# Kernel tuning notes

Hardware: AMD Instinct MI355X
Metric: run time of the kernel (lower is better)

The kernel has to match this reference:

```python
import jax, jax.numpy as jnp
import numpy as np

B, S, E, H, D = 384, 128, 512, 4, 128  # batch, seq(block), embed, heads, head_dim


def setup_inputs() -> dict:
    key = jax.random.key(0)
    ks = jax.random.split(key, 6)
    scale = 1.0 / np.sqrt(E)  # lecun_normal-ish fan-in scaling
    return {
        "x": jax.random.normal(ks[0], (B, S, E), dtype=jnp.float32),
        "Wq": jax.random.normal(ks[1], (E, E), dtype=jnp.float32) * scale,
        "bq": jnp.zeros((E,), dtype=jnp.float32),
        "Wk": jax.random.normal(ks[2], (E, E), dtype=jnp.float32) * scale,
        "bk": jnp.zeros((E,), dtype=jnp.float32),
        "Wv": jax.random.normal(ks[3], (E, E), dtype=jnp.float32) * scale,
        "bv": jnp.zeros((E,), dtype=jnp.float32),
        "Wo": jax.random.normal(ks[4], (E, E), dtype=jnp.float32) * scale,
        "bo": jnp.zeros((E,), dtype=jnp.float32),
    }


def reference(x, Wq, bq, Wk, bk, Wv, bv, Wo, bo):
    # Projections, then split heads: [B,S,E] -> [B,S,H,D]
    q = (x @ Wq + bq).reshape(B, S, H, D)
    k = (x @ Wk + bk).reshape(B, S, H, D)
    v = (x @ Wv + bv).reshape(B, S, H, D)
    # NOTE: original applies no 1/sqrt(D) scaling and no mask.
    scores = jnp.einsum("BSHD,BTHD->BHST", q, k)  # [B,H,S,T]
    weights = jax.nn.softmax(scores, axis=-1)
    out = jnp.einsum("BHST,BTHD->BSHD", weights, v).reshape(B, S, E)
    return out @ Wo + bo
```

## Files before the change

kernel.cpp:

```cpp
#include <hip/hip_runtime.h>
#include <hip/hip_bf16.h>
#include <cstdint>


#define EMB 512

typedef __attribute__((ext_vector_type(4))) float    f32x4;
typedef __attribute__((ext_vector_type(8))) _Float16 f16x8;

#define MFMA16(a, b, c) __builtin_amdgcn_mfma_f32_16x16x32_f16((a), (b), (c), 0, 0, 0)

__device__ __forceinline__ int swz128(int row, int col) {
    return row * 128 + (col ^ (((row >> 2) & 3) << 4));
}
__device__ __forceinline__ int swz64(int row, int col) {
    return row * 64 + (col ^ (((row >> 2) & 3) << 4));
}

__device__ __forceinline__ void gld_lds16(const _Float16* g, _Float16* l) {
    __builtin_amdgcn_global_load_lds(
        (const __attribute__((address_space(1))) void*)g,
        (__attribute__((address_space(3))) void*)l, 16, 0, 0);
}

__device__ __forceinline__ void stage64(_Float16* lds, const _Float16* gbase,
                                        int grow0, int k0, int wave, int lane) {
#pragma unroll
    for (int i = 0; i < 4; ++i) {
        int idx = wave * 256 + i * 64 + lane;
        int n   = idx >> 3;
        int kb  = (idx & 7) ^ (((n >> 2) & 3) << 1);
        gld_lds16(gbase + (grow0 + n) * EMB + k0 + kb * 8,
                  lds + wave * 2048 + i * 512);
    }
}

__device__ __forceinline__ void proj_gemm(f32x4 acc[2][8],
        const _Float16* __restrict__ abase, int arow0,
        const _Float16* __restrict__ sbase, int srow0,
        _Float16* stageL, int wave, int lane) {
    const int l15 = lane & 15, quad = lane >> 4;
    for (int k0 = 0; k0 < EMB; k0 += 64) {
        stage64(stageL, sbase, srow0, k0, wave, lane);
        __syncthreads();
#pragma unroll
        for (int ktl = 0; ktl < 2; ++ktl) {
            int kk = k0 + ktl * 32 + quad * 8;
            f16x8 a0 = *(const f16x8*)(abase + (arow0 + l15) * EMB + kk);
            f16x8 a1 = *(const f16x8*)(abase + (arow0 + 16 + l15) * EMB + kk);
#pragma unroll
            for (int nt = 0; nt < 8; ++nt) {
                int n = nt * 16 + l15;
                int c = (ktl * 32 + quad * 8) ^ (((n >> 2) & 3) << 4);
                f16x8 bb = *(const f16x8*)(stageL + n * 64 + c);
                acc[0][nt] = MFMA16(a0, bb, acc[0][nt]);
                acc[1][nt] = MFMA16(a1, bb, acc[1][nt]);
            }
        }
        __syncthreads();
    }
}

#define ZACC(A)                                   \
    _Pragma("unroll") for (int _i = 0; _i < 2; ++_i) \
    _Pragma("unroll") for (int _j = 0; _j < 8; ++_j) \
        A[_i][_j] = (f32x4){0.f, 0.f, 0.f, 0.f};

__global__ void k_cvt_x(const float* __restrict__ x, _Float16* __restrict__ xh) {
    long i = ((long)blockIdx.x * 256 + threadIdx.x) * 8;
    f32x4 a = *(const f32x4*)(x + i);
    f32x4 b = *(const f32x4*)(x + i + 4);
    f16x8 o;
    o[0] = (_Float16)a[0]; o[1] = (_Float16)a[1];
    o[2] = (_Float16)a[2]; o[3] = (_Float16)a[3];
    o[4] = (_Float16)b[0]; o[5] = (_Float16)b[1];
    o[6] = (_Float16)b[2]; o[7] = (_Float16)b[3];
    *(f16x8*)(xh + i) = o;
}

__global__ void k_transpose_w(const float* __restrict__ W, _Float16* __restrict__ Wt) {
    __shared__ float t[32][33];
    int tid = threadIdx.x;
    int tx = tid & 31, ty = tid >> 5;
    int k0 = blockIdx.x * 32, n0 = blockIdx.y * 32;
#pragma unroll
    for (int i = 0; i < 4; ++i)
        t[ty + i * 8][tx] = W[(k0 + ty + i * 8) * EMB + n0 + tx];
    __syncthreads();
#pragma unroll
    for (int i = 0; i < 4; ++i)
        Wt[(n0 + ty + i * 8) * EMB + k0 + tx] = (_Float16)t[tx][ty + i * 8];
}

__global__ __launch_bounds__(256, 2)
void k_attn(const _Float16* __restrict__ xh,
            const _Float16* __restrict__ Wqt, const _Float16* __restrict__ Wkt,
            const _Float16* __restrict__ Wvt,
            const float* __restrict__ bq, const float* __restrict__ bk,
            const float* __restrict__ bv,
            _Float16* __restrict__ attn) {
    __shared__ _Float16 RA[128 * 128];
    __shared__ _Float16 RB[128 * 128];
    const int tid = threadIdx.x, wave = tid >> 6, lane = tid & 63;
    const int l15 = lane & 15, quad = lane >> 4;
    const int b = blockIdx.x >> 2, h = blockIdx.x & 3;
    const int sRow0 = b * 128, wRow0 = h * 128;
    f32x4 acc[2][8];

    ZACC(acc);
    proj_gemm(acc, xh, sRow0 + wave * 32, Wqt, wRow0, RB, wave, lane);
#pragma unroll
    for (int mt = 0; mt < 2; ++mt)
#pragma unroll
        for (int nt = 0; nt < 8; ++nt) {
            int col = nt * 16 + l15;
            float bias = bq[wRow0 + col];
#pragma unroll
            for (int r = 0; r < 4; ++r) {
                int row = wave * 32 + mt * 16 + quad * 4 + r;
                RA[swz128(row, col)] = (_Float16)(acc[mt][nt][r] + bias);
            }
        }

    ZACC(acc);
    proj_gemm(acc, xh, sRow0 + wave * 32, Wkt, wRow0, RB, wave, lane);
#pragma unroll
    for (int mt = 0; mt < 2; ++mt)
#pragma unroll
        for (int nt = 0; nt < 8; ++nt) {
            int col = nt * 16 + l15;
            float bias = bk[wRow0 + col];
#pragma unroll
            for (int r = 0; r < 4; ++r) {
                int row = wave * 32 + mt * 16 + quad * 4 + r;
                RB[swz128(row, col)] = (_Float16)(acc[mt][nt][r] + bias);
            }
        }
    __syncthreads();

    ZACC(acc);
#pragma unroll
    for (int kt = 0; kt < 4; ++kt) {
        int ca = kt * 32 + quad * 8;
        int rq = wave * 32 + l15;
        f16x8 q0 = *(const f16x8*)&RA[swz128(rq, ca)];
        f16x8 q1 = *(const f16x8*)&RA[swz128(rq + 16, ca)];
#pragma unroll
        for (int nt = 0; nt < 8; ++nt) {
            f16x8 kf = *(const f16x8*)&RB[swz128(nt * 16 + l15, ca)];
            acc[0][nt] = MFMA16(q0, kf, acc[0][nt]);
            acc[1][nt] = MFMA16(q1, kf, acc[1][nt]);
        }
    }
#pragma unroll
    for (int mt = 0; mt < 2; ++mt)
#pragma unroll
        for (int r = 0; r < 4; ++r) {
            float mx = acc[mt][0][r];
#pragma unroll
            for (int nt = 1; nt < 8; ++nt) mx = fmaxf(mx, acc[mt][nt][r]);
            mx = fmaxf(mx, __shfl_xor(mx, 1));
            mx = fmaxf(mx, __shfl_xor(mx, 2));
            mx = fmaxf(mx, __shfl_xor(mx, 4));
            mx = fmaxf(mx, __shfl_xor(mx, 8));
            float sm = 0.f;
#pragma unroll
            for (int nt = 0; nt < 8; ++nt) {
                float e = __expf(acc[mt][nt][r] - mx);
                acc[mt][nt][r] = e;
                sm += e;
            }
            sm += __shfl_xor(sm, 1);
            sm += __shfl_xor(sm, 2);
            sm += __shfl_xor(sm, 4);
            sm += __shfl_xor(sm, 8);
            float inv = 1.0f / sm;
#pragma unroll
            for (int nt = 0; nt < 8; ++nt) acc[mt][nt][r] *= inv;
        }
    __syncthreads();

#pragma unroll
    for (int mt = 0; mt < 2; ++mt)
#pragma unroll
        for (int nt = 0; nt < 8; ++nt) {
            int col = nt * 16 + l15;
#pragma unroll
            for (int r = 0; r < 4; ++r) {
                int row = wave * 32 + mt * 16 + quad * 4 + r;
                RA[swz128(row, col)] = (_Float16)acc[mt][nt][r];
            }
        }

    ZACC(acc);
    proj_gemm(acc, Wvt, wRow0 + wave * 32, xh, sRow0, RB, wave, lane);
#pragma unroll
    for (int mt = 0; mt < 2; ++mt)
#pragma unroll
        for (int r = 0; r < 4; ++r) {
            int row = wave * 32 + mt * 16 + quad * 4 + r;
            float bias = bv[wRow0 + row];
#pragma unroll
            for (int nt = 0; nt < 8; ++nt) {
                int col = nt * 16 + l15;
                RB[swz128(row, col)] = (_Float16)(acc[mt][nt][r] + bias);
            }
        }
    __syncthreads();

    ZACC(acc);
#pragma unroll
    for (int kt = 0; kt < 4; ++kt) {
        int ca = kt * 32 + quad * 8;
        int rp = wave * 32 + l15;
        f16x8 p0 = *(const f16x8*)&RA[swz128(rp, ca)];
        f16x8 p1 = *(const f16x8*)&RA[swz128(rp + 16, ca)];
#pragma unroll
        for (int nt = 0; nt < 8; ++nt) {
            f16x8 vf = *(const f16x8*)&RB[swz128(nt * 16 + l15, ca)];
            acc[0][nt] = MFMA16(p0, vf, acc[0][nt]);
            acc[1][nt] = MFMA16(p1, vf, acc[1][nt]);
        }
    }
    __syncthreads();

#pragma unroll
    for (int mt = 0; mt < 2; ++mt)
#pragma unroll
        for (int nt = 0; nt < 8; ++nt) {
            int col = nt * 16 + l15;
#pragma unroll
            for (int r = 0; r < 4; ++r) {
                int row = wave * 32 + mt * 16 + quad * 4 + r;
                RA[swz128(row, col)] = (_Float16)acc[mt][nt][r];
            }
        }
    __syncthreads();
#pragma unroll
    for (int i = 0; i < 8; ++i) {
        int idx = i * 256 + tid;
        int row = idx >> 4, col = (idx & 15) * 8;
        f16x8 v = *(const f16x8*)&RA[row * 128 + (col ^ (((row >> 2) & 3) << 4))];
        *(f16x8*)(attn + (long)(sRow0 + row) * EMB + wRow0 + col) = v;
    }
}

__global__ __launch_bounds__(256, 3)
void k_out(const _Float16* __restrict__ attn, const _Float16* __restrict__ Wot,
           const float* __restrict__ bo, float* __restrict__ out) {
    __shared__ _Float16 SA[128 * 64];
    __shared__ _Float16 SB[128 * 64];
    const int tid = threadIdx.x, wave = tid >> 6, lane = tid & 63;
    const int l15 = lane & 15, quad = lane >> 4;
    const int m0 = (blockIdx.x >> 2) * 128, n0 = (blockIdx.x & 3) * 128;
    f32x4 acc[2][8];
    ZACC(acc);
    for (int k0 = 0; k0 < EMB; k0 += 64) {
        stage64(SA, attn, m0, k0, wave, lane);
        stage64(SB, Wot, n0, k0, wave, lane);
        __syncthreads();
#pragma unroll
        for (int ktl = 0; ktl < 2; ++ktl) {
            int ra = wave * 32 + l15;
            int cb = ktl * 32 + quad * 8;
            f16x8 a0 = *(const f16x8*)&SA[swz64(ra, cb)];
            f16x8 a1 = *(const f16x8*)&SA[swz64(ra + 16, cb)];
#pragma unroll
            for (int nt = 0; nt < 8; ++nt) {
                f16x8 bb = *(const f16x8*)&SB[swz64(nt * 16 + l15, cb)];
                acc[0][nt] = MFMA16(a0, bb, acc[0][nt]);
                acc[1][nt] = MFMA16(a1, bb, acc[1][nt]);
            }
        }
        __syncthreads();
    }
#pragma unroll
    for (int nt = 0; nt < 8; ++nt) {
        int col = n0 + nt * 16 + l15;
        float bias = bo[col];
#pragma unroll
        for (int mt = 0; mt < 2; ++mt)
#pragma unroll
            for (int r = 0; r < 4; ++r) {
                int row = m0 + wave * 32 + mt * 16 + quad * 4 + r;
                out[(long)row * EMB + col] = acc[mt][nt][r] + bias;
            }
    }
}

extern "C" void kernel_launch(void* const* d_in, const int* in_sizes, int n_in,
                              void* d_out, int out_size, void* d_ws, size_t ws_size,
                              hipStream_t stream) {
    const float* x  = (const float*)d_in[0];
    const float* Wq = (const float*)d_in[1];
    const float* bq = (const float*)d_in[2];
    const float* Wk = (const float*)d_in[3];
    const float* bk = (const float*)d_in[4];
    const float* Wv = (const float*)d_in[5];
    const float* bv = (const float*)d_in[6];
    const float* Wo = (const float*)d_in[7];
    const float* bo = (const float*)d_in[8];
    float* out = (float*)d_out;

    _Float16* xh   = (_Float16*)d_ws;
    _Float16* Wqt  = (_Float16*)((char*)d_ws + 50331648);
    _Float16* Wkt  = Wqt + 262144;
    _Float16* Wvt  = Wkt + 262144;
    _Float16* Wot  = Wvt + 262144;
    _Float16* attn = Wot + 262144;

    k_cvt_x<<<12288, 256, 0, stream>>>(x, xh);
    dim3 tg(16, 16);
    k_transpose_w<<<tg, 256, 0, stream>>>(Wq, Wqt);
    k_transpose_w<<<tg, 256, 0, stream>>>(Wk, Wkt);
    k_transpose_w<<<tg, 256, 0, stream>>>(Wv, Wvt);
    k_transpose_w<<<tg, 256, 0, stream>>>(Wo, Wot);
    k_attn<<<1536, 256, 0, stream>>>(xh, Wqt, Wkt, Wvt, bq, bk, bv, attn);
    k_out<<<1536, 256, 0, stream>>>(attn, Wot, bo, out);
}
```

Baseline: 411.3 us.

## Split fused attention into a standalone QKV GEMM kernel and an attention-core kernel

Moves the Q/K/V projections out of the fused attention kernel into a separate GEMM kernel over a concatenated QKV weight. That kernel stages both operands in LDS and writes Q and K row-major and V transposed per head to global scratch. The attention core then only loads K and V^T tiles into LDS, reads Q from global, and does the softmax and PV. The old fused kernel read the A operand straight from global and ran serialized per-head projections. The split adds a round trip of Q/K/V through HBM (about 150MB) and an extra launch. It also raises k_out's occupancy hint to 4.

```diff
diff --git a/kernel.cpp b/kernel.cpp
--- a/kernel.cpp
+++ b/kernel.cpp
@@ -35,29 +35,16 @@
     }
 }
 
-__device__ __forceinline__ void proj_gemm(f32x4 acc[2][8],
-        const _Float16* __restrict__ abase, int arow0,
-        const _Float16* __restrict__ sbase, int srow0,
-        _Float16* stageL, int wave, int lane) {
-    const int l15 = lane & 15, quad = lane >> 4;
-    for (int k0 = 0; k0 < EMB; k0 += 64) {
-        stage64(stageL, sbase, srow0, k0, wave, lane);
-        __syncthreads();
-#pragma unroll
-        for (int ktl = 0; ktl < 2; ++ktl) {
-            int kk = k0 + ktl * 32 + quad * 8;
-            f16x8 a0 = *(const f16x8*)(abase + (arow0 + l15) * EMB + kk);
-            f16x8 a1 = *(const f16x8*)(abase + (arow0 + 16 + l15) * EMB + kk);
-#pragma unroll
-            for (int nt = 0; nt < 8; ++nt) {
-                int n = nt * 16 + l15;
-                int c = (ktl * 32 + quad * 8) ^ (((n >> 2) & 3) << 4);
-                f16x8 bb = *(const f16x8*)(stageL + n * 64 + c);
-                acc[0][nt] = MFMA16(a0, bb, acc[0][nt]);
-                acc[1][nt] = MFMA16(a1, bb, acc[1][nt]);
-            }
-        }
-        __syncthreads();
+__device__ __forceinline__ void stage128(_Float16* lds, const _Float16* gbase,
+                                         long grow0, int gstride, int gcol0,
+                                         int wave, int lane) {
+#pragma unroll
+    for (int i = 0; i < 8; ++i) {
+        int idx = wave * 512 + i * 64 + lane;
+        int n   = idx >> 4;
+        int kb  = (idx & 15) ^ (((n >> 2) & 3) << 1);
+        gld_lds16(gbase + (grow0 + n) * gstride + gcol0 + kb * 8,
+                  lds + wave * 4096 + i * 512);
     }
 }
 
@@ -92,62 +79,102 @@
         Wt[(n0 + ty + i * 8) * EMB + k0 + tx] = (_Float16)t[tx][ty + i * 8];
 }
 
+__global__ __launch_bounds__(256, 4)
+void k_qkv(const _Float16* __restrict__ xh, const _Float16* __restrict__ Wqkvt,
+           const float* __restrict__ bq, const float* __restrict__ bk,
+           const float* __restrict__ bv,
+           _Float16* __restrict__ qb, _Float16* __restrict__ kb,
+           _Float16* __restrict__ vtb) {
+    __shared__ _Float16 SA[128 * 64];
+    __shared__ _Float16 SB[128 * 64];
+    const int tid = threadIdx.x, wave = tid >> 6, lane = tid & 63;
+    const int l15 = lane & 15, quad = lane >> 4;
+    const int bi = blockIdx.x;
+    const int bb = bi / 12, j = bi - bb * 12;
+    const int m0 = bb * 128;
+    const bool vswap = (j >= 8);
+    const _Float16* As = vswap ? SB : SA;
+    const _Float16* Bs = vswap ? SA : SB;
+    f32x4 acc[2][8];
+    ZACC(acc);
+    for (int k0 = 0; k0 < EMB; k0 += 64) {
+        stage64(SA, xh, m0, k0, wave, lane);
+        stage64(SB, Wqkvt, j * 128, k0, wave, lane);
+        __syncthreads();
+#pragma unroll
+        for (int ktl = 0; ktl < 2; ++ktl) {
+            int cb = ktl * 32 + quad * 8;
+            f16x8 a0 = *(const f16x8*)&As[swz64(wave * 32 + l15, cb)];
+            f16x8 a1 = *(const f16x8*)&As[swz64(wave * 32 + 16 + l15, cb)];
+#pragma unroll
+            for (int nt = 0; nt < 8; ++nt) {
+                f16x8 bbf = *(const f16x8*)&Bs[swz64(nt * 16 + l15, cb)];
+                acc[0][nt] = MFMA16(a0, bbf, acc[0][nt]);
+                acc[1][nt] = MFMA16(a1, bbf, acc[1][nt]);
+            }
+        }
+        __syncthreads();
+    }
+    if (!vswap) {
+        const float* bias = (j < 4) ? bq : bk;
+        _Float16* dst = (j < 4) ? qb : kb;
+        const int nc0 = (j & 3) * 128;
+#pragma unroll
+        for (int nt = 0; nt < 8; ++nt) {
+            int col = nt * 16 + l15;
+            float bv_ = bias[nc0 + col];
+#pragma unroll
+            for (int mt = 0; mt < 2; ++mt)
+#pragma unroll
+                for (int r = 0; r < 4; ++r) {
+                    int row = wave * 32 + mt * 16 + quad * 4 + r;
+                    dst[(long)(m0 + row) * EMB + nc0 + col] =
+                        (_Float16)(acc[mt][nt][r] + bv_);
+                }
+        }
+    } else {
+        const int hv = j - 8;
+        _Float16* dst = vtb + (long)(bb * 4 + hv) * 128 * 128;
+#pragma unroll
+        for (int mt = 0; mt < 2; ++mt)
+#pragma unroll
+            for (int r = 0; r < 4; ++r) {
+                int d = wave * 32 + mt * 16 + quad * 4 + r;
+                float bvv = bv[hv * 128 + d];
+#pragma unroll
+                for (int nt = 0; nt < 8; ++nt) {
+                    int t = nt * 16 + l15;
+                    dst[d * 128 + t] = (_Float16)(acc[mt][nt][r] + bvv);
+                }
+            }
+    }
+}
+
 __global__ __launch_bounds__(256, 2)
-void k_attn(const _Float16* __restrict__ xh,
-            const _Float16* __restrict__ Wqt, const _Float16* __restrict__ Wkt,
-            const _Float16* __restrict__ Wvt,
-            const float* __restrict__ bq, const float* __restrict__ bk,
-            const float* __restrict__ bv,
-            _Float16* __restrict__ attn) {
-    __shared__ _Float16 RA[128 * 128];
-    __shared__ _Float16 RB[128 * 128];
+void k_core(const _Float16* __restrict__ qb, const _Float16* __restrict__ kb,
+            const _Float16* __restrict__ vtb, _Float16* __restrict__ attn) {
+    __shared__ _Float16 SK[128 * 128];
+    __shared__ _Float16 SV[128 * 128];
     const int tid = threadIdx.x, wave = tid >> 6, lane = tid & 63;
     const int l15 = lane & 15, quad = lane >> 4;
     const int b = blockIdx.x >> 2, h = blockIdx.x & 3;
     const int sRow0 = b * 128, wRow0 = h * 128;
     f32x4 acc[2][8];
 
-    ZACC(acc);
-    proj_gemm(acc, xh, sRow0 + wave * 32, Wqt, wRow0, RB, wave, lane);
-#pragma unroll
-    for (int mt = 0; mt < 2; ++mt)
-#pragma unroll
-        for (int nt = 0; nt < 8; ++nt) {
-            int col = nt * 16 + l15;
-            float bias = bq[wRow0 + col];
-#pragma unroll
-            for (int r = 0; r < 4; ++r) {
-                int row = wave * 32 + mt * 16 + quad * 4 + r;
-                RA[swz128(row, col)] = (_Float16)(acc[mt][nt][r] + bias);
-            }
-        }
-
-    ZACC(acc);
-    proj_gemm(acc, xh, sRow0 + wave * 32, Wkt, wRow0, RB, wave, lane);
-#pragma unroll
-    for (int mt = 0; mt < 2; ++mt)
-#pragma unroll
-        for (int nt = 0; nt < 8; ++nt) {
-            int col = nt * 16 + l15;
-            float bias = bk[wRow0 + col];
-#pragma unroll
-            for (int r = 0; r < 4; ++r) {
-                int row = wave * 32 + mt * 16 + quad * 4 + r;
-                RB[swz128(row, col)] = (_Float16)(acc[mt][nt][r] + bias);
-            }
-        }
+    stage128(SK, kb, sRow0, EMB, wRow0, wave, lane);
+    stage128(SV, vtb, (long)(b * 4 + h) * 128, 128, 0, wave, lane);
     __syncthreads();
 
     ZACC(acc);
 #pragma unroll
     for (int kt = 0; kt < 4; ++kt) {
         int ca = kt * 32 + quad * 8;
-        int rq = wave * 32 + l15;
-        f16x8 q0 = *(const f16x8*)&RA[swz128(rq, ca)];
-        f16x8 q1 = *(const f16x8*)&RA[swz128(rq + 16, ca)];
-#pragma unroll
-        for (int nt = 0; nt < 8; ++nt) {
-            f16x8 kf = *(const f16x8*)&RB[swz128(nt * 16 + l15, ca)];
+        const _Float16* qrow = qb + (long)(sRow0 + wave * 32 + l15) * EMB + wRow0 + ca;
+        f16x8 q0 = *(const f16x8*)qrow;
+        f16x8 q1 = *(const f16x8*)(qrow + 16 * EMB);
+#pragma unroll
+        for (int nt = 0; nt < 8; ++nt) {
+            f16x8 kf = *(const f16x8*)&SK[swz128(nt * 16 + l15, ca)];
             acc[0][nt] = MFMA16(q0, kf, acc[0][nt]);
             acc[1][nt] = MFMA16(q1, kf, acc[1][nt]);
         }
@@ -188,22 +215,7 @@
 #pragma unroll
             for (int r = 0; r < 4; ++r) {
                 int row = wave * 32 + mt * 16 + quad * 4 + r;
-                RA[swz128(row, col)] = (_Float16)acc[mt][nt][r];
-            }
-        }
-
-    ZACC(acc);
-    proj_gemm(acc, Wvt, wRow0 + wave * 32, xh, sRow0, RB, wave, lane);
-#pragma unroll
-    for (int mt = 0; mt < 2; ++mt)
-#pragma unroll
-        for (int r = 0; r < 4; ++r) {
-            int row = wave * 32 + mt * 16 + quad * 4 + r;
-            float bias = bv[wRow0 + row];
-#pragma unroll
-            for (int nt = 0; nt < 8; ++nt) {
-                int col = nt * 16 + l15;
-                RB[swz128(row, col)] = (_Float16)(acc[mt][nt][r] + bias);
+                SK[swz128(row, col)] = (_Float16)acc[mt][nt][r];
             }
         }
     __syncthreads();
@@ -213,11 +225,11 @@
     for (int kt = 0; kt < 4; ++kt) {
         int ca = kt * 32 + quad * 8;
         int rp = wave * 32 + l15;
-        f16x8 p0 = *(const f16x8*)&RA[swz128(rp, ca)];
-        f16x8 p1 = *(const f16x8*)&RA[swz128(rp + 16, ca)];
-#pragma unroll
-        for (int nt = 0; nt < 8; ++nt) {
-            f16x8 vf = *(const f16x8*)&RB[swz128(nt * 16 + l15, ca)];
+        f16x8 p0 = *(const f16x8*)&SK[swz128(rp, ca)];
+        f16x8 p1 = *(const f16x8*)&SK[swz128(rp + 16, ca)];
+#pragma unroll
+        for (int nt = 0; nt < 8; ++nt) {
+            f16x8 vf = *(const f16x8*)&SV[swz128(nt * 16 + l15, ca)];
             acc[0][nt] = MFMA16(p0, vf, acc[0][nt]);
             acc[1][nt] = MFMA16(p1, vf, acc[1][nt]);
         }
@@ -232,7 +244,7 @@
 #pragma unroll
             for (int r = 0; r < 4; ++r) {
                 int row = wave * 32 + mt * 16 + quad * 4 + r;
-                RA[swz128(row, col)] = (_Float16)acc[mt][nt][r];
+                SK[swz128(row, col)] = (_Float16)acc[mt][nt][r];
             }
         }
     __syncthreads();
@@ -240,12 +252,12 @@
     for (int i = 0; i < 8; ++i) {
         int idx = i * 256 + tid;
         int row = idx >> 4, col = (idx & 15) * 8;
-        f16x8 v = *(const f16x8*)&RA[row * 128 + (col ^ (((row >> 2) & 3) << 4))];
+        f16x8 v = *(const f16x8*)&SK[row * 128 + (col ^ (((row >> 2) & 3) << 4))];
         *(f16x8*)(attn + (long)(sRow0 + row) * EMB + wRow0 + col) = v;
     }
 }
 
-__global__ __launch_bounds__(256, 3)
+__global__ __launch_bounds__(256, 4)
 void k_out(const _Float16* __restrict__ attn, const _Float16* __restrict__ Wot,
            const float* __restrict__ bo, float* __restrict__ out) {
     __shared__ _Float16 SA[128 * 64];
@@ -302,19 +314,22 @@
     const float* bo = (const float*)d_in[8];
     float* out = (float*)d_out;
 
-    _Float16* xh   = (_Float16*)d_ws;
-    _Float16* Wqt  = (_Float16*)((char*)d_ws + 50331648);
-    _Float16* Wkt  = Wqt + 262144;
-    _Float16* Wvt  = Wkt + 262144;
-    _Float16* Wot  = Wvt + 262144;
-    _Float16* attn = Wot + 262144;
+    char* w = (char*)d_ws;
+    _Float16* xh    = (_Float16*)(w);
+    _Float16* attn  = xh;
+    _Float16* Wqkvt = (_Float16*)(w + 50331648);
+    _Float16* Wot   = (_Float16*)(w + 51904512);
+    _Float16* qb    = (_Float16*)(w + 52428800);
+    _Float16* kb    = (_Float16*)(w + 102760448);
+    _Float16* vtb   = (_Float16*)(w + 153092096);
 
     k_cvt_x<<<12288, 256, 0, stream>>>(x, xh);
     dim3 tg(16, 16);
-    k_transpose_w<<<tg, 256, 0, stream>>>(Wq, Wqt);
-    k_transpose_w<<<tg, 256, 0, stream>>>(Wk, Wkt);
-    k_transpose_w<<<tg, 256, 0, stream>>>(Wv, Wvt);
+    k_transpose_w<<<tg, 256, 0, stream>>>(Wq, Wqkvt);
+    k_transpose_w<<<tg, 256, 0, stream>>>(Wk, Wqkvt + 512 * EMB);
+    k_transpose_w<<<tg, 256, 0, stream>>>(Wv, Wqkvt + 1024 * EMB);
     k_transpose_w<<<tg, 256, 0, stream>>>(Wo, Wot);
-    k_attn<<<1536, 256, 0, stream>>>(xh, Wqt, Wkt, Wvt, bq, bk, bv, attn);
+    k_qkv<<<4608, 256, 0, stream>>>(xh, Wqkvt, bq, bk, bv, qb, kb, vtb);
+    k_core<<<1536, 256, 0, stream>>>(qb, kb, vtb, attn);
     k_out<<<1536, 256, 0, stream>>>(attn, Wot, bo, out);
 }
```

New measurement: 385.3 us. 6.3% less time.
